# Performance work log

Measured on AMD Instinct MI355X. Metric: run time of the kernel, lower is better.

## Reference

```python
import jax, jax.numpy as jnp
import numpy as np

N_NODES = 20000
N_EDGES = 480000
NUM_BATCH = 8     # B = batch_id.max()+1 (static)
NUM_GLOBAL = 3    # virtual_frame_num default
NUM_RBF = 16
EPS = 1e-20


def make_frames(n, ca, c):
    """OpenFold Rigid.make_transform_from_reference. Returns (R [N,3,3], t [N,3])."""
    nl = n - ca
    cl = c - ca
    cx, cy, cz = cl[:, 0], cl[:, 1], cl[:, 2]
    norm1 = jnp.sqrt(EPS + cx * cx + cy * cy)
    s1, c1 = -cy / norm1, cx / norm1
    norm2 = jnp.sqrt(EPS + cx * cx + cy * cy + cz * cz)
    s2, c2 = cz / norm2, jnp.sqrt(cx * cx + cy * cy) / norm2
    z = jnp.zeros_like(c1)
    o = jnp.ones_like(c1)
    R1 = jnp.stack([jnp.stack([c1, -s1, z], -1),
                    jnp.stack([s1, c1, z], -1),
                    jnp.stack([z, z, o], -1)], -2)          # rot about z
    R2 = jnp.stack([jnp.stack([c2, z, s2], -1),
                    jnp.stack([z, o, z], -1),
                    jnp.stack([-s2, z, c2], -1)], -2)       # rot about y
    Rc = jnp.einsum('nij,njk->nik', R2, R1)
    nr = jnp.einsum('nij,nj->ni', Rc, nl)
    ny, nz = nr[:, 1], nr[:, 2]
    norm3 = jnp.sqrt(EPS + ny * ny + nz * nz)
    sn, cn = -nz / norm3, ny / norm3
    Rn = jnp.stack([jnp.stack([o, z, z], -1),
                    jnp.stack([z, cn, -sn], -1),
                    jnp.stack([z, sn, cn], -1)], -2)        # rot about x
    R = jnp.einsum('nij,njk->nik', Rn, Rc).swapaxes(-1, -2)
    return R, ca


def rbf_encode(D):
    # D_min=0, D_max=20, 16 bins (matches rbf_func)
    mu = jnp.linspace(0.0, 20.0, NUM_RBF, dtype=D.dtype)
    sigma = 20.0 / NUM_RBF
    z = (D[..., None] - mu) / sigma
    return jnp.exp(-z * z)


def decouple(U):
    # safe norm: exact forward, NaN-free backward at U==0
    sq = jnp.sum(U * U, axis=-1, keepdims=True)
    norm = jnp.where(sq == 0, 0.0, jnp.sqrt(jnp.where(sq == 0, 1.0, sq)))
    direct = U / (norm + 1e-6)
    return jnp.concatenate([direct, rbf_encode(norm[..., 0])], axis=-1)


def int_embedding(d, num_embeddings):
    freq = jnp.exp(jnp.arange(0, num_embeddings, 2, dtype=jnp.float32)
                   * (-np.log(10000.0) / num_embeddings))
    ang = d[:, None].astype(jnp.float32) * freq[None, :]
    return jnp.concatenate([jnp.cos(ang), jnp.sin(ang)], -1)


def forward(X, edge_idx, batch_id, chain_encoding):
    N = X.shape[0]
    src, dst = edge_idx[0], edge_idx[1]
    R, t = make_frames(X[:, 0], X[:, 1], X[:, 2])
    # T_ts = T[dst].invert().compose(T[src]):  R_dst^T R_src,  R_dst^T (t_src - t_dst)
    R_ts = jnp.einsum('eji,ejk->eik', R[dst], R[src])
    t_ts = jnp.einsum('eji,ej->ei', R[dst], t[src] - t[dst])
    # --- node features ---
    diffX = jnp.diff(X.reshape(-1, 3), axis=0)
    diffX = jnp.concatenate([jnp.zeros((1, 3), X.dtype), diffX], 0).reshape(N, 4, 3)
    diffX_proj = jnp.einsum('nji,naj->nai', R, diffX)   # R^T @ diffX
    V = decouple(diffX_proj).reshape(N, -1)             # [N, 4*(3+16)=76]
    V = jnp.where(jnp.isnan(V), 0.0, V)
    # --- edge features ---
    atoms = jnp.concatenate([X[src], X[dst]], axis=1)   # [E,8,3]
    diffE = jnp.einsum('eji,eaj->eai', R[src], atoms - t[src][:, None, :])
    diffE = decouple(diffE).reshape(src.shape[0], -1)   # [E,152]
    pos_embed = int_embedding(src - dst, 16)            # [E,16]
    E_quant = R_ts.swapaxes(-1, -2).reshape(-1, 9)      # inverted rot mats
    E_trans = decouple(t_ts)                            # [E,19]
    Efeat = jnp.concatenate([diffE, E_quant, E_trans, pos_embed], -1)  # [E,196]
    # --- virtual (global) frames ---
    B, G = NUM_BATCH, NUM_GLOBAL
    g_src = jnp.concatenate([batch_id + N + k * B for k in range(G)])  # [G*N]
    g_dst = jnp.tile(jnp.arange(N, dtype=edge_idx.dtype), G)
    edge_idx_g = jnp.concatenate([jnp.stack([g_src, g_dst]),
                                  jnp.stack([g_dst, g_src])], axis=1)  # [2, 2*G*N]
    batch_id_g = jnp.tile(jnp.arange(B, dtype=batch_id.dtype), G)      # [G*B]
    h_V_g = jnp.tile(jnp.arange(G), B)                                 # [G*B]
    V_g = int_embedding(h_V_g, V.shape[-1]).astype(V.dtype)            # [G*B,76]
    n_ge = edge_idx_g.shape[1]
    E_g = jnp.zeros((n_ge, Efeat.shape[1]), Efeat.dtype)
    eye = jnp.eye(3, dtype=X.dtype)
    # --- merge local + global ---
    V_all = jnp.concatenate([V, V_g], 0)
    E_all = jnp.concatenate([Efeat, E_g], 0)
    R_all = jnp.concatenate([R, jnp.broadcast_to(eye, (G * B, 3, 3))], 0)
    t_all = jnp.concatenate([t, jnp.zeros((G * B, 3), X.dtype)], 0)
    Rts_all = jnp.concatenate([R_ts, jnp.broadcast_to(eye, (n_ge, 3, 3))], 0)
    tts_all = jnp.concatenate([t_ts, jnp.zeros((n_ge, 3), X.dtype)], 0)
    batch_all = jnp.concatenate([batch_id, batch_id_g])
    edge_all = jnp.concatenate([edge_idx, edge_idx_g], axis=1)
    chain_all = jnp.concatenate([chain_encoding, jnp.ones_like(batch_id_g) + 1000])
    return V_all, E_all, R_all, t_all, Rts_all, tts_all, batch_all, edge_all, chain_all


def setup_inputs() -> dict:
    key = jax.random.key(0)
    k1, k2, k3, k4 = jax.random.split(key, 4)
    X = jax.random.normal(k1, (N_NODES, 4, 3), dtype=jnp.float32)
    edge_idx = jax.random.randint(k2, (2, N_EDGES), 0, N_NODES, dtype=jnp.int32)
    batch_id = jnp.sort(jax.random.randint(k3, (N_NODES,), 0, NUM_BATCH, dtype=jnp.int32))
    chain_encoding = jax.random.randint(k4, (N_NODES,), 0, 10, dtype=jnp.int32)
    return {"X": X, "edge_idx": edge_idx, "batch_id": batch_id,
            "chain_encoding": chain_encoding}


def reference(X, edge_idx, batch_id, chain_encoding):
    return forward(X, edge_idx, batch_id, chain_encoding)
```

## Files before the change

### kernel.cpp

```cpp
#include <hip/hip_runtime.h>

#define NN 20000
#define NE 480000

#define OFF_V    0
#define OFF_E    1521824
#define OFF_R    119121824
#define OFF_T    119302040
#define OFF_RTS  119362112
#define OFF_TTS  124762112
#define OFF_BAT  126562112
#define OFF_EDG  126582136
#define OFF_CHN  127782136

#define REC 65

#define NB_EDGE 3750
#define NB_NODE 157
#define NB_FILL 3064
#define NB_TOTAL (NB_EDGE + NB_NODE + NB_FILL)

#define ZQUOTA 1592
#define ZSEG_A 5880000

struct Frame { float m[3][3]; float t[3]; };

__device__ __forceinline__ void make_frame(const float a0[3], const float a1[3],
                                           const float a2[3], Frame& F){
  float nlx = a0[0]-a1[0], nly = a0[1]-a1[1], nlz = a0[2]-a1[2];
  float cx  = a2[0]-a1[0], cy  = a2[1]-a1[1], cz  = a2[2]-a1[2];
  float xy2 = cx*cx + cy*cy;
  float n1 = sqrtf(1e-20f + xy2);
  float s1 = -cy/n1, c1 = cx/n1;
  float n2 = sqrtf(1e-20f + xy2 + cz*cz);
  float s2 = cz/n2, c2 = sqrtf(xy2)/n2;
  float R00 = c2*c1, R01 = -c2*s1, R02 = s2;
  float R10 = s1,    R11 = c1,     R12 = 0.f;
  float R20 = -s2*c1,R21 = s2*s1,  R22 = c2;
  float nr1 = R10*nlx + R11*nly + R12*nlz;
  float nr2 = R20*nlx + R21*nly + R22*nlz;
  float n3 = sqrtf(1e-20f + nr1*nr1 + nr2*nr2);
  float sn = -nr2/n3, cn = nr1/n3;
  F.m[0][0]=R00;              F.m[0][1]=R01;              F.m[0][2]=R02;
  F.m[1][0]=cn*R10 - sn*R20;  F.m[1][1]=cn*R11 - sn*R21;  F.m[1][2]=cn*R12 - sn*R22;
  F.m[2][0]=sn*R10 + cn*R20;  F.m[2][1]=sn*R11 + cn*R21;  F.m[2][2]=sn*R12 + cn*R22;
  F.t[0]=a1[0]; F.t[1]=a1[1]; F.t[2]=a1[2];
}

__device__ __forceinline__ void group4(float ux, float uy, float uz, float* rec, int off){
  float sq = ux*ux + uy*uy + uz*uz;
  float nrm = (sq == 0.f) ? 0.f : sqrtf(sq);
  float inv = 1.0f / (nrm + 1e-6f);
  rec[off+0] = ux*inv; rec[off+1] = uy*inv; rec[off+2] = uz*inv; rec[off+3] = nrm;
}

__device__ __forceinline__ void decouple19(float ux, float uy, float uz, float* b){
  float sq = ux*ux + uy*uy + uz*uz;
  float nrm = (sq == 0.f) ? 0.f : sqrtf(sq);
  float inv = 1.0f / (nrm + 1e-6f);
  b[0] = ux*inv; b[1] = uy*inv; b[2] = uz*inv;
#pragma unroll
  for (int k = 0; k < 16; k++){
    float mu = (float)k * (20.0f/15.0f);
    float z = (nrm - mu) * 0.8f;
    b[3+k] = __expf(-z*z);
  }
}

__global__ __launch_bounds__(128) void mega_kernel(
    const float* __restrict__ X, const int* __restrict__ ei,
    const int* __restrict__ bat, const int* __restrict__ chn,
    float* __restrict__ out){
  __shared__ float lds[2*64*REC];
  const int blk = blockIdx.x;
  const int tid = threadIdx.x;

  if (blk < NB_EDGE){
    const int lane = tid & 63;
    const int wave = tid >> 6;
    const int e_my = blk*128 + tid;

    {
      const int zbase = blk * ZQUOTA;
      uint4 zz; zz.x=0; zz.y=0; zz.z=0; zz.w=0;
#pragma unroll
      for (int k = 0; k < 13; k++){
        int zi = k*128 + tid;
        if (zi < ZQUOTA){
          int gidx = zbase + zi;
          if (gidx < ZSEG_A)
            reinterpret_cast<uint4*>(out + 95601824)[gidx] = zz;
          else
            reinterpret_cast<uint4*>(out + 126202112)[gidx - ZSEG_A] = zz;
        }
      }
    }

    int src = ei[e_my], dst = ei[NE + e_my];
    const float* ps = X + (size_t)src*12;
    const float* pd = X + (size_t)dst*12;
    float as[4][3], ad[4][3];
#pragma unroll
    for (int i = 0; i < 12; i++){ as[i/3][i%3] = ps[i]; ad[i/3][i%3] = pd[i]; }
    Frame Fs, Fd;
    make_frame(as[0], as[1], as[2], Fs);
    make_frame(ad[0], ad[1], ad[2], Fd);

    float* rec = lds + (wave*64 + lane)*REC;

#pragma unroll
    for (int q = 0; q < 4; q++){
      float y0 = as[q][0]-Fs.t[0], y1 = as[q][1]-Fs.t[1], y2 = as[q][2]-Fs.t[2];
      group4(Fs.m[0][0]*y0 + Fs.m[0][1]*y1 + Fs.m[0][2]*y2,
             Fs.m[1][0]*y0 + Fs.m[1][1]*y1 + Fs.m[1][2]*y2,
             Fs.m[2][0]*y0 + Fs.m[2][1]*y1 + Fs.m[2][2]*y2, rec, 4*q);
    }
#pragma unroll
    for (int q = 0; q < 4; q++){
      float y0 = ad[q][0]-Fs.t[0], y1 = ad[q][1]-Fs.t[1], y2 = ad[q][2]-Fs.t[2];
      group4(Fs.m[0][0]*y0 + Fs.m[0][1]*y1 + Fs.m[0][2]*y2,
             Fs.m[1][0]*y0 + Fs.m[1][1]*y1 + Fs.m[1][2]*y2,
             Fs.m[2][0]*y0 + Fs.m[2][1]*y1 + Fs.m[2][2]*y2, rec, 16 + 4*q);
    }
#pragma unroll
    for (int i = 0; i < 3; i++)
#pragma unroll
      for (int k = 0; k < 3; k++)
        rec[36+3*i+k] = Fd.m[i][0]*Fs.m[k][0] + Fd.m[i][1]*Fs.m[k][1] + Fd.m[i][2]*Fs.m[k][2];
    {
      float d0 = Fs.t[0]-Fd.t[0], d1 = Fs.t[1]-Fd.t[1], d2 = Fs.t[2]-Fd.t[2];
      float t0 = Fd.m[0][0]*d0 + Fd.m[0][1]*d1 + Fd.m[0][2]*d2;
      float t1 = Fd.m[1][0]*d0 + Fd.m[1][1]*d1 + Fd.m[1][2]*d2;
      float t2 = Fd.m[2][0]*d0 + Fd.m[2][1]*d1 + Fd.m[2][2]*d2;
      rec[45] = t0; rec[46] = t1; rec[47] = t2;
      group4(t0, t1, t2, rec, 32);
    }
    {
      float df = (float)(src - dst);
      const float FR[8] = {1.f, 0.31622776601683794f, 0.1f, 0.031622776601683794f,
                           0.01f, 0.0031622776601683794f, 0.001f, 0.00031622776601683794f};
#pragma unroll
      for (int k = 0; k < 8; k++){
        float s, c; __sincosf(df * FR[k], &s, &c);
        rec[48+k] = c; rec[56+k] = s;
      }
    }
    out[OFF_EDG + e_my]          = (float)src;
    out[OFF_EDG + 600000 + e_my] = (float)dst;


    int   offb[4];
    float msk[4], mu[4];
#pragma unroll
    for (int c = 0; c < 4; c++){
      int j = 4*lane + c;
      int off = 0; float m = 0.f, rm = 0.f;
      if (j < 152){
        int jj = (j < 76) ? j : j - 76;
        int gq = ((j < 76) ? 0 : 4) + jj/19;
        int r  = jj - 19*(jj/19);
        if (r < 3) off = 4*gq + r;
        else { off = 4*gq + 3; m = 1.f; rm = (float)(r-3) * (20.0f/15.0f); }
      } else if (j < 161){
        int q = j - 152;
        off = 36 + 3*(q - 3*(q/3)) + q/3;
      } else if (j < 180){
        int r = j - 161;
        if (r < 3) off = 32 + r;
        else { off = 35; m = 1.f; rm = (float)(r-3) * (20.0f/15.0f); }
      } else if (j < 196){
        off = 48 + (j - 180);
      } else {
        off = 0;
      }
      offb[c] = off; msk[c] = m; mu[c] = rm;
    }

    const float* wlds = lds + wave*64*REC;
    const int wave_ebase = blk*128 + wave*64;
    float4* pstore = reinterpret_cast<float4*>(out + OFF_E + (size_t)wave_ebase*196) + lane;

#pragma unroll 2
    for (int e = 0; e < 64; e++){
      const float* r = wlds + e*REC;
      float v[4];
#pragma unroll
      for (int c = 0; c < 4; c++){
        float x  = r[offb[c]];
        float z  = (x - mu[c]) * 0.8f;
        float rv = __expf(-z*z);
        v[c] = fmaf(msk[c], rv - x, x);
      }
      if (lane < 49)
        *pstore = make_float4(v[0], v[1], v[2], v[3]);
      pstore += 49;
    }

#pragma unroll
    for (int k = 0; k < 9; k++){
      int f = k*64 + lane;
      int e = f/9, m = f - 9*e;
      out[OFF_RTS + (size_t)wave_ebase*9 + f] = wlds[e*REC + 36 + m];
    }
#pragma unroll
    for (int k = 0; k < 3; k++){
      int f = k*64 + lane;
      int e = f/3, m = f - 3*e;
      out[OFF_TTS + (size_t)wave_ebase*3 + f] = wlds[e*REC + 45 + m];
    }
    return;
  }

  if (blk < NB_EDGE + NB_NODE){
    int n = (blk - NB_EDGE)*128 + tid;
    if (n >= NN) return;
    const float* xp = X + (size_t)n*12;
    float a[4][3];
#pragma unroll
    for (int i = 0; i < 12; i++) a[i/3][i%3] = xp[i];
    Frame F; make_frame(a[0], a[1], a[2], F);

    float d[4][3];
    if (n > 0){ d[0][0]=a[0][0]-xp[-3]; d[0][1]=a[0][1]-xp[-2]; d[0][2]=a[0][2]-xp[-1]; }
    else      { d[0][0]=0.f; d[0][1]=0.f; d[0][2]=0.f; }
#pragma unroll
    for (int q = 1; q < 4; q++){
      d[q][0]=a[q][0]-a[q-1][0]; d[q][1]=a[q][1]-a[q-1][1]; d[q][2]=a[q][2]-a[q-1][2];
    }

    float buf[76];
#pragma unroll
    for (int q = 0; q < 4; q++){
      float vx = F.m[0][0]*d[q][0] + F.m[0][1]*d[q][1] + F.m[0][2]*d[q][2];
      float vy = F.m[1][0]*d[q][0] + F.m[1][1]*d[q][1] + F.m[1][2]*d[q][2];
      float vz = F.m[2][0]*d[q][0] + F.m[2][1]*d[q][1] + F.m[2][2]*d[q][2];
      decouple19(vx, vy, vz, buf + q*19);
    }
    float4* vrow = reinterpret_cast<float4*>(out + OFF_V + (size_t)n*76);
#pragma unroll
    for (int i = 0; i < 19; i++)
      vrow[i] = make_float4(buf[4*i], buf[4*i+1], buf[4*i+2], buf[4*i+3]);

    float* rr = out + OFF_R + (size_t)n*9;
#pragma unroll
    for (int i = 0; i < 3; i++)
#pragma unroll
      for (int j = 0; j < 3; j++) rr[3*i+j] = F.m[j][i];

    float* tr = out + OFF_T + (size_t)n*3;
#pragma unroll
    for (int i = 0; i < 3; i++) tr[i] = F.t[i];

    out[OFF_BAT + n] = (float)bat[n];
    out[OFF_CHN + n] = (float)chn[n];
    return;
  }

  int i = (blk - NB_EDGE - NB_NODE)*128 + tid;
  if (i < 270000){
    float v[4];
#pragma unroll
    for (int c = 0; c < 4; c++){
      int idx = 4*i + c;
      int r = idx % 9;
      v[c] = (r==0 || r==4 || r==8) ? 1.0f : 0.0f;
    }
    reinterpret_cast<float4*>(out + OFF_RTS + 4320000)[i] = make_float4(v[0],v[1],v[2],v[3]);
    return;
  }
  i -= 270000;
  if (i < 120000){
    int v0, v1;
    if (i < 60000){ int k = i/20000, m = i - 20000*k; v0 = bat[m] + 20000 + k*8; v1 = m; }
    else { int i2 = i - 60000; int k = i2/20000, m = i2 - 20000*k; v0 = m; v1 = bat[m] + 20000 + k*8; }
    out[OFF_EDG + 480000 + i]          = (float)v0;
    out[OFF_EDG + 600000 + 480000 + i] = (float)v1;
    return;
  }
  i -= 120000;
  if (i >= 2160) return;
  if (i < 1824){
    int r = i / 76, c = i % 76;
    float hv = (float)(r % 3);
    int j = (c < 38) ? c : c - 38;
    float fr = __expf(-(float)(2*j) * (9.210340371976184f/76.0f));
    float ang = hv * fr;
    out[OFF_V + 1520000 + i] = (c < 38) ? cosf(ang) : sinf(ang);
  } else if (i < 2040){
    int k = i - 1824; int r = k % 9;
    out[OFF_R + 180000 + k] = (r==0 || r==4 || r==8) ? 1.0f : 0.0f;
  } else if (i < 2112){
    out[OFF_T + 60000 + (i - 2040)] = 0.0f;
  } else if (i < 2136){
    int k = i - 2112;
    out[OFF_BAT + 20000 + k] = (float)(k % 8);
  } else {
    out[OFF_CHN + 20000 + (i - 2136)] = 1001.0f;
  }
}

extern "C" void kernel_launch(void* const* d_in, const int* in_sizes, int n_in,
                              void* d_out, int out_size, void* d_ws, size_t ws_size,
                              hipStream_t stream) {
  const float* X   = (const float*)d_in[0];
  const int* ei    = (const int*)d_in[1];
  const int* bat   = (const int*)d_in[2];
  const int* chn   = (const int*)d_in[3];
  float* out = (float*)d_out;

  mega_kernel<<<NB_TOTAL, 128, 0, stream>>>(X, ei, bat, chn, out);
}
```

Before: 115.6 us.

## Repack edge feature store loop to use all lanes and shrink LDS records

The per-edge output loop now spreads the 45 float4 columns of the 64 edges in a wave across all 64 lanes, using per-wave LDS tables of offsets and RBF centres, instead of having 15 lanes idle per edge. The sinusoidal positional features are computed in a separate store pass directly from the stored index difference, which shrinks each LDS record from 65 to 49 floats. This targets wasted lanes and LDS footprint, at the cost of extra LDS table reads and integer division per element.

```diff
diff --git a/kernel.cpp b/kernel.cpp
--- a/kernel.cpp
+++ b/kernel.cpp
@@ -13,7 +13,7 @@
 #define OFF_EDG  126582136
 #define OFF_CHN  127782136
 
-#define REC 65
+#define REC 49
 
 #define NB_EDGE 3750
 #define NB_NODE 157
@@ -71,7 +71,9 @@
     const float* __restrict__ X, const int* __restrict__ ei,
     const int* __restrict__ bat, const int* __restrict__ chn,
     float* __restrict__ out){
-  __shared__ float lds[2*64*REC];
+  __shared__ float  lds[2*64*REC];
+  __shared__ int4   moff[2][45];
+  __shared__ float4 mmu[2][45];
   const int blk = blockIdx.x;
   const int tid = threadIdx.x;
 
@@ -135,65 +137,88 @@
       rec[45] = t0; rec[46] = t1; rec[47] = t2;
       group4(t0, t1, t2, rec, 32);
     }
-    {
-      float df = (float)(src - dst);
-      const float FR[8] = {1.f, 0.31622776601683794f, 0.1f, 0.031622776601683794f,
-                           0.01f, 0.0031622776601683794f, 0.001f, 0.00031622776601683794f};
-#pragma unroll
-      for (int k = 0; k < 8; k++){
-        float s, c; __sincosf(df * FR[k], &s, &c);
-        rec[48+k] = c; rec[56+k] = s;
-      }
-    }
+    rec[48] = (float)(src - dst);
+
+    if (lane < 45){
+      int   o[4], fl[4];
+      float rm[4];
+#pragma unroll
+      for (int c = 0; c < 4; c++){
+        int j = 4*lane + c;
+        int off = 0, flag = 0; float m = 0.f;
+        if (j < 152){
+          int jj = (j < 76) ? j : j - 76;
+          int gq = ((j < 76) ? 0 : 4) + jj/19;
+          int r  = jj - 19*(jj/19);
+          if (r < 3) off = 4*gq + r;
+          else { off = 4*gq + 3; flag = 1; m = (float)(r-3) * (20.0f/15.0f); }
+        } else if (j < 161){
+          int q = j - 152;
+          off = 36 + 3*(q - 3*(q/3)) + q/3;
+        } else {
+          int r = j - 161;
+          if (r < 3) off = 32 + r;
+          else { off = 35; flag = 1; m = (float)(r-3) * (20.0f/15.0f); }
+        }
+        o[c] = off | (flag << 8); fl[c] = flag; rm[c] = m;
+      }
+      moff[wave][lane] = make_int4(o[0], o[1], o[2], o[3]);
+      mmu[wave][lane]  = make_float4(rm[0], rm[1], rm[2], rm[3]);
+      (void)fl;
+    }
+
     out[OFF_EDG + e_my]          = (float)src;
     out[OFF_EDG + 600000 + e_my] = (float)dst;
 
 
-    int   offb[4];
-    float msk[4], mu[4];
-#pragma unroll
-    for (int c = 0; c < 4; c++){
-      int j = 4*lane + c;
-      int off = 0; float m = 0.f, rm = 0.f;
-      if (j < 152){
-        int jj = (j < 76) ? j : j - 76;
-        int gq = ((j < 76) ? 0 : 4) + jj/19;
-        int r  = jj - 19*(jj/19);
-        if (r < 3) off = 4*gq + r;
-        else { off = 4*gq + 3; m = 1.f; rm = (float)(r-3) * (20.0f/15.0f); }
-      } else if (j < 161){
-        int q = j - 152;
-        off = 36 + 3*(q - 3*(q/3)) + q/3;
-      } else if (j < 180){
-        int r = j - 161;
-        if (r < 3) off = 32 + r;
-        else { off = 35; m = 1.f; rm = (float)(r-3) * (20.0f/15.0f); }
-      } else if (j < 196){
-        off = 48 + (j - 180);
-      } else {
-        off = 0;
-      }
-      offb[c] = off; msk[c] = m; mu[c] = rm;
-    }
-
     const float* wlds = lds + wave*64*REC;
     const int wave_ebase = blk*128 + wave*64;
-    float4* pstore = reinterpret_cast<float4*>(out + OFF_E + (size_t)wave_ebase*196) + lane;
-
-#pragma unroll 2
-    for (int e = 0; e < 64; e++){
-      const float* r = wlds + e*REC;
+
+#pragma unroll 5
+    for (int it = 0; it < 45; it++){
+      int f   = it*64 + lane;
+      int row = f / 45;
+      int j4  = f - 45*row;
+      const float* r = wlds + row*REC;
+      int4   op = moff[wave][j4];
+      float4 mv = mmu[wave][j4];
       float v[4];
+      {
+        float x = r[op.x & 0xFF]; float z = (x - mv.x)*0.8f;
+        float rv = __expf(-z*z);  v[0] = (op.x >> 8) ? rv : x;
+      }
+      {
+        float x = r[op.y & 0xFF]; float z = (x - mv.y)*0.8f;
+        float rv = __expf(-z*z);  v[1] = (op.y >> 8) ? rv : x;
+      }
+      {
+        float x = r[op.z & 0xFF]; float z = (x - mv.z)*0.8f;
+        float rv = __expf(-z*z);  v[2] = (op.z >> 8) ? rv : x;
+      }
+      {
+        float x = r[op.w & 0xFF]; float z = (x - mv.w)*0.8f;
+        float rv = __expf(-z*z);  v[3] = (op.w >> 8) ? rv : x;
+      }
+      float4* p = reinterpret_cast<float4*>(out + OFF_E + (size_t)(wave_ebase + row)*196) + j4;
+      *p = make_float4(v[0], v[1], v[2], v[3]);
+    }
+
+#pragma unroll
+    for (int it = 0; it < 4; it++){
+      int f   = it*64 + lane;
+      int row = f >> 2;
+      int t   = f & 3;
+      float df = wlds[row*REC + 48];
+      float v[4];
 #pragma unroll
       for (int c = 0; c < 4; c++){
-        float x  = r[offb[c]];
-        float z  = (x - mu[c]) * 0.8f;
-        float rv = __expf(-z*z);
-        v[c] = fmaf(msk[c], rv - x, x);
-      }
-      if (lane < 49)
-        *pstore = make_float4(v[0], v[1], v[2], v[3]);
-      pstore += 49;
+        int e8 = 4*t + c;
+        float fq = exp2f(-(float)(e8 & 7) * 1.6609640474436813f);
+        float s, co; __sincosf(df * fq, &s, &co);
+        v[c] = (e8 < 8) ? co : s;
+      }
+      float4* p = reinterpret_cast<float4*>(out + OFF_E + (size_t)(wave_ebase + row)*196 + 180) + t;
+      *p = make_float4(v[0], v[1], v[2], v[3]);
     }
 
 #pragma unroll
```

New measurement: 157.7 us. 36.4% more time.
